# Kernel tuning notes

Measured on AMD Instinct MI355X. Metric: run time of the kernel, lower is better.

Reference implementation:

```python
import jax, jax.numpy as jnp
import numpy as np

# Dims: B=batch, C=in_ch (channels), L=pooled length, N=num_classes
B, C, L, N = 256, 2048, 512, 1000
FINAL_SHIFT = 4            # final_shift init arg
FC_SHIFT = 11              # int(log2(in_ch)) = int(log2(2048))


def dead_shift(x_i32, shift):
    # zero out values with |x| < 2^shift, then arithmetic right shift
    thr = jnp.int32(1 << shift)
    x = jnp.where(jnp.abs(x_i32) >= thr, x_i32, jnp.int32(0))
    return x >> shift  # numpy-style arithmetic shift for signed int32


def shift_clamp_i32_to_i8(x_i32, shift):
    x = dead_shift(x_i32, shift)
    return jnp.clip(x, -128, 127).astype(jnp.int8)


def setup_inputs() -> dict:
    key = jax.random.key(0)
    k1, k2 = jax.random.split(key)
    x = jax.random.randint(k1, (B, C, L), -128, 128, dtype=jnp.int32).astype(jnp.int8)
    weights = jax.random.randint(k2, (N, C), -128, 128, dtype=jnp.int32).astype(jnp.int8)
    return {"x": x, "weights": weights}


def reference(x, weights):
    # sum-pool over L: (B, C, L) -> (B, C) in int32
    acc = jnp.sum(x.astype(jnp.int32), axis=2)
    acc = dead_shift(acc, FINAL_SHIFT)
    # IntLinear: int32 matmul (same math as the torch broadcast-multiply-sum,
    # without materializing the (B, N, C) intermediate)
    w32 = weights.astype(jnp.int32)
    y = jnp.einsum('bc,nc->bn', acc, w32)  # (B, N) int32
    return shift_clamp_i32_to_i8(y, FC_SHIFT)
```

## Files before the change

### kernel.cpp

```cpp
#include <hip/hip_runtime.h>

#define BB 256
#define CC 2048
#define LL 512
#define NN 1000
#define FINAL_SHIFT 4
#define FC_SHIFT 11

#define TB 32
#define TN 64
#define BK 64

__device__ __forceinline__ int dead_shift_i(int x, int shift) {
    int thr = 1 << shift;
    int ax = x < 0 ? -x : x;
    x = (ax >= thr) ? x : 0;
    return x >> shift;
}

__global__ __launch_bounds__(256) void pool_kernel(const int* __restrict__ x,
                                                   int* __restrict__ acc) {
    int wave = threadIdx.x >> 6;
    int lane = threadIdx.x & 63;
    int g    = lane >> 4;
    int j    = lane & 15;
    long long rowBase = ((long long)blockIdx.x * 4 + wave) * 4;
    const int* p = x + (rowBase + g) * (long long)LL;

    int4 v[8];
#pragma unroll
    for (int c = 0; c < 8; ++c)
        v[c] = *(const int4*)(p + c * 64 + j * 4);

    int s = 0;
#pragma unroll
    for (int c = 0; c < 8; ++c) s += v[c].x + v[c].y + v[c].z + v[c].w;

    s += __shfl_xor(s, 1, 64);
    s += __shfl_xor(s, 2, 64);
    s += __shfl_xor(s, 4, 64);
    s += __shfl_xor(s, 8, 64);

    if (j == 0) acc[rowBase + g] = dead_shift_i(s, FINAL_SHIFT);
}

__global__ __launch_bounds__(256) void gemm_kernel(const int* __restrict__ acc,
                                                   const int* __restrict__ w,
                                                   int* __restrict__ partial,
                                                   int kch) {
    __shared__ int As[TB][BK + 1];
    __shared__ int Ws[BK][TN + 4];

    int b0 = blockIdx.x * TB;
    int n0 = blockIdx.y * TN;
    int kbase = blockIdx.z * kch;

    int t  = threadIdx.x;
    int tx = t & 15;
    int ty = t >> 4;

    int r[2][4] = {{0, 0, 0, 0}, {0, 0, 0, 0}};

    for (int k0 = kbase; k0 < kbase + kch; k0 += BK) {
        {
            int idx = t * 8;
            int b   = idx >> 6;
            int kk  = idx & 63;
            const int* src = acc + (long long)(b0 + b) * CC + k0 + kk;
            int4 u0 = *(const int4*)(src);
            int4 u1 = *(const int4*)(src + 4);
            As[b][kk + 0] = u0.x; As[b][kk + 1] = u0.y;
            As[b][kk + 2] = u0.z; As[b][kk + 3] = u0.w;
            As[b][kk + 4] = u1.x; As[b][kk + 5] = u1.y;
            As[b][kk + 6] = u1.z; As[b][kk + 7] = u1.w;
        }
#pragma unroll
        for (int rep = 0; rep < 4; ++rep) {
            int n  = rep * 16 + ty;
            int kk = tx * 4;
            int nn = n0 + n;
            int4 u = make_int4(0, 0, 0, 0);
            if (nn < NN) u = *(const int4*)(w + (long long)nn * CC + k0 + kk);
            Ws[kk + 0][n] = u.x; Ws[kk + 1][n] = u.y;
            Ws[kk + 2][n] = u.z; Ws[kk + 3][n] = u.w;
        }
        __syncthreads();

#pragma unroll
        for (int kk = 0; kk < BK; ++kk) {
            int4 wv = *(const int4*)&Ws[kk][tx * 4];
            int a0 = As[ty * 2 + 0][kk];
            int a1 = As[ty * 2 + 1][kk];
            r[0][0] += a0 * wv.x; r[0][1] += a0 * wv.y; r[0][2] += a0 * wv.z; r[0][3] += a0 * wv.w;
            r[1][0] += a1 * wv.x; r[1][1] += a1 * wv.y; r[1][2] += a1 * wv.z; r[1][3] += a1 * wv.w;
        }
        __syncthreads();
    }

    long long base = (long long)blockIdx.z * BB * NN;
#pragma unroll
    for (int i = 0; i < 2; ++i) {
#pragma unroll
        for (int j = 0; j < 4; ++j) {
            int n = n0 + tx * 4 + j;
            if (n < NN)
                partial[base + (long long)(b0 + ty * 2 + i) * NN + n] = r[i][j];
        }
    }
}

__global__ __launch_bounds__(256) void epilogue_kernel(const int* __restrict__ partial,
                                                       int* __restrict__ out, int z) {
    int idx = blockIdx.x * 256 + threadIdx.x;
    if (idx >= BB * NN) return;
    int s = 0;
    for (int i = 0; i < z; ++i) s += partial[(long long)i * BB * NN + idx];
    int v = dead_shift_i(s, FC_SHIFT);
    v = min(127, max(-128, v));
    out[idx] = v;
}

extern "C" void kernel_launch(void* const* d_in, const int* in_sizes, int n_in,
                              void* d_out, int out_size, void* d_ws, size_t ws_size,
                              hipStream_t stream) {
    const int* x = (const int*)d_in[0];
    const int* w = (const int*)d_in[1];
    int* out = (int*)d_out;

    int* acc     = (int*)d_ws;
    int* partial = acc + (size_t)BB * CC;

    size_t need4 = ((size_t)BB * CC + 4ull * BB * NN) * 4;
    int Z = (ws_size >= need4) ? 4 : 1;
    int kch = CC / Z;

    pool_kernel<<<(BB * CC) / 16, 256, 0, stream>>>(x, acc);

    dim3 g2(BB / TB, (NN + TN - 1) / TN, Z);
    gemm_kernel<<<g2, 256, 0, stream>>>(acc, w, partial, kch);

    epilogue_kernel<<<(BB * NN + 255) / 256, 256, 0, stream>>>(partial, out, Z);
}
```

Before: 236.1 us.

## Enlarge GEMM register tile, swizzle LDS, deepen split-K and double pool rows

The GEMM tile grows from 32x64 to 64x128, with a 4x8 per-thread register tile. A-tile stores to LDS are vectorised, and the W tile uses an XOR swizzle to reduce bank conflicts. Multiplies switch to __mul24, which is safe here because the pooled values and weights fit in 24 bits. Split-K now goes up to 16 chunks when workspace allows, and the pool kernel sums 8 rows per wave instead of 4 for more memory-level parallelism. The trade-off is more partial-sum traffic in the epilogue and higher register pressure in the GEMM.

```diff
diff --git a/kernel.cpp b/kernel.cpp
--- a/kernel.cpp
+++ b/kernel.cpp
@@ -7,9 +7,11 @@
 #define FINAL_SHIFT 4
 #define FC_SHIFT 11
 
-#define TB 32
-#define TN 64
+#define TBB 64
+#define TNN 128
 #define BK 64
+#define AP 76
+#define WP 132
 
 __device__ __forceinline__ int dead_shift_i(int x, int shift) {
     int thr = 1 << shift;
@@ -22,89 +24,128 @@
                                                    int* __restrict__ acc) {
     int wave = threadIdx.x >> 6;
     int lane = threadIdx.x & 63;
-    int g    = lane >> 4;
-    int j    = lane & 15;
-    long long rowBase = ((long long)blockIdx.x * 4 + wave) * 4;
-    const int* p = x + (rowBase + g) * (long long)LL;
+    int g = lane >> 4;
+    int j = lane & 15;
+    long long rowBase = ((long long)blockIdx.x * 4 + wave) * 8;
+    const int* pA = x + (rowBase + g) * (long long)LL;
+    const int* pB = x + (rowBase + 4 + g) * (long long)LL;
 
-    int4 v[8];
+    int4 v[8], u[8];
 #pragma unroll
-    for (int c = 0; c < 8; ++c)
-        v[c] = *(const int4*)(p + c * 64 + j * 4);
+    for (int c = 0; c < 8; ++c) v[c] = *(const int4*)(pA + c * 64 + j * 4);
+#pragma unroll
+    for (int c = 0; c < 8; ++c) u[c] = *(const int4*)(pB + c * 64 + j * 4);
 
-    int s = 0;
+    int sA = 0, sB = 0;
 #pragma unroll
-    for (int c = 0; c < 8; ++c) s += v[c].x + v[c].y + v[c].z + v[c].w;
+    for (int c = 0; c < 8; ++c) sA += v[c].x + v[c].y + v[c].z + v[c].w;
+#pragma unroll
+    for (int c = 0; c < 8; ++c) sB += u[c].x + u[c].y + u[c].z + u[c].w;
 
-    s += __shfl_xor(s, 1, 64);
-    s += __shfl_xor(s, 2, 64);
-    s += __shfl_xor(s, 4, 64);
-    s += __shfl_xor(s, 8, 64);
+    sA += __shfl_xor(sA, 1, 64);  sB += __shfl_xor(sB, 1, 64);
+    sA += __shfl_xor(sA, 2, 64);  sB += __shfl_xor(sB, 2, 64);
+    sA += __shfl_xor(sA, 4, 64);  sB += __shfl_xor(sB, 4, 64);
+    sA += __shfl_xor(sA, 8, 64);  sB += __shfl_xor(sB, 8, 64);
 
-    if (j == 0) acc[rowBase + g] = dead_shift_i(s, FINAL_SHIFT);
+    if (j == 0) {
+        acc[rowBase + g]     = dead_shift_i(sA, FINAL_SHIFT);
+        acc[rowBase + 4 + g] = dead_shift_i(sB, FINAL_SHIFT);
+    }
 }
 
 __global__ __launch_bounds__(256) void gemm_kernel(const int* __restrict__ acc,
                                                    const int* __restrict__ w,
                                                    int* __restrict__ partial,
                                                    int kch) {
-    __shared__ int As[TB][BK + 1];
-    __shared__ int Ws[BK][TN + 4];
+    __shared__ int As[TBB][AP];
+    __shared__ int Ws[BK][WP];
 
-    int b0 = blockIdx.x * TB;
-    int n0 = blockIdx.y * TN;
+    int b0 = blockIdx.x * TBB;
+    int n0 = blockIdx.y * TNN;
     int kbase = blockIdx.z * kch;
 
     int t  = threadIdx.x;
     int tx = t & 15;
     int ty = t >> 4;
 
-    int r[2][4] = {{0, 0, 0, 0}, {0, 0, 0, 0}};
+    int r[4][8];
+#pragma unroll
+    for (int bi = 0; bi < 4; ++bi)
+#pragma unroll
+        for (int j = 0; j < 8; ++j) r[bi][j] = 0;
 
     for (int k0 = kbase; k0 < kbase + kch; k0 += BK) {
         {
-            int idx = t * 8;
-            int b   = idx >> 6;
-            int kk  = idx & 63;
-            const int* src = acc + (long long)(b0 + b) * CC + k0 + kk;
-            int4 u0 = *(const int4*)(src);
+            int b  = t >> 2;
+            int kq = (t & 3) * 16;
+            const int* src = acc + (long long)(b0 + b) * CC + k0 + kq;
+            int4 u0 = *(const int4*)(src + 0);
             int4 u1 = *(const int4*)(src + 4);
-            As[b][kk + 0] = u0.x; As[b][kk + 1] = u0.y;
-            As[b][kk + 2] = u0.z; As[b][kk + 3] = u0.w;
-            As[b][kk + 4] = u1.x; As[b][kk + 5] = u1.y;
-            As[b][kk + 6] = u1.z; As[b][kk + 7] = u1.w;
+            int4 u2 = *(const int4*)(src + 8);
+            int4 u3 = *(const int4*)(src + 12);
+            *(int4*)&As[b][kq + 0]  = u0;
+            *(int4*)&As[b][kq + 4]  = u1;
+            *(int4*)&As[b][kq + 8]  = u2;
+            *(int4*)&As[b][kq + 12] = u3;
         }
+        {
+            int kk = tx * 4;
+            int sw = ((tx >> 1) & 3) << 2;
 #pragma unroll
-        for (int rep = 0; rep < 4; ++rep) {
-            int n  = rep * 16 + ty;
-            int kk = tx * 4;
-            int nn = n0 + n;
-            int4 u = make_int4(0, 0, 0, 0);
-            if (nn < NN) u = *(const int4*)(w + (long long)nn * CC + k0 + kk);
-            Ws[kk + 0][n] = u.x; Ws[kk + 1][n] = u.y;
-            Ws[kk + 2][n] = u.z; Ws[kk + 3][n] = u.w;
+            for (int rep = 0; rep < 8; ++rep) {
+                int n  = rep * 16 + ty;
+                int nn = n0 + n;
+                int4 uw = make_int4(0, 0, 0, 0);
+                if (nn < NN) uw = *(const int4*)(w + (long long)nn * CC + k0 + kk);
+                int c = n ^ sw;
+                Ws[kk + 0][c] = uw.x;
+                Ws[kk + 1][c] = uw.y;
+                Ws[kk + 2][c] = uw.z;
+                Ws[kk + 3][c] = uw.w;
+            }
         }
         __syncthreads();
 
 #pragma unroll
-        for (int kk = 0; kk < BK; ++kk) {
-            int4 wv = *(const int4*)&Ws[kk][tx * 4];
-            int a0 = As[ty * 2 + 0][kk];
-            int a1 = As[ty * 2 + 1][kk];
-            r[0][0] += a0 * wv.x; r[0][1] += a0 * wv.y; r[0][2] += a0 * wv.z; r[0][3] += a0 * wv.w;
-            r[1][0] += a1 * wv.x; r[1][1] += a1 * wv.y; r[1][2] += a1 * wv.z; r[1][3] += a1 * wv.w;
+        for (int kk4 = 0; kk4 < BK; kk4 += 4) {
+            int4 a[4];
+#pragma unroll
+            for (int bi = 0; bi < 4; ++bi)
+                a[bi] = *(const int4*)&As[ty * 4 + bi][kk4];
+#pragma unroll
+            for (int uu = 0; uu < 4; ++uu) {
+                int kk  = kk4 + uu;
+                int swr = ((kk >> 3) & 3) << 2;
+                int c0  = (tx * 4) ^ swr;
+                int4 w0 = *(const int4*)&Ws[kk][c0];
+                int4 w1 = *(const int4*)&Ws[kk][64 + c0];
+#pragma unroll
+                for (int bi = 0; bi < 4; ++bi) {
+                    int av = (uu == 0) ? a[bi].x : (uu == 1) ? a[bi].y
+                           : (uu == 2) ? a[bi].z : a[bi].w;
+                    r[bi][0] += __mul24(av, w0.x);
+                    r[bi][1] += __mul24(av, w0.y);
+                    r[bi][2] += __mul24(av, w0.z);
+                    r[bi][3] += __mul24(av, w0.w);
+                    r[bi][4] += __mul24(av, w1.x);
+                    r[bi][5] += __mul24(av, w1.y);
+                    r[bi][6] += __mul24(av, w1.z);
+                    r[bi][7] += __mul24(av, w1.w);
+                }
+            }
         }
         __syncthreads();
     }
 
     long long base = (long long)blockIdx.z * BB * NN;
 #pragma unroll
-    for (int i = 0; i < 2; ++i) {
+    for (int bi = 0; bi < 4; ++bi) {
+        int b = b0 + ty * 4 + bi;
 #pragma unroll
-        for (int j = 0; j < 4; ++j) {
-            int n = n0 + tx * 4 + j;
+        for (int j = 0; j < 8; ++j) {
+            int n = n0 + ((j < 4) ? (tx * 4 + j) : (64 + tx * 4 + (j - 4)));
             if (n < NN)
-                partial[base + (long long)(b0 + ty * 2 + i) * NN + n] = r[i][j];
+                partial[base + (long long)b * NN + n] = r[bi][j];
         }
     }
 }
@@ -130,13 +171,14 @@
     int* acc     = (int*)d_ws;
     int* partial = acc + (size_t)BB * CC;
 
-    size_t need4 = ((size_t)BB * CC + 4ull * BB * NN) * 4;
-    int Z = (ws_size >= need4) ? 4 : 1;
+    size_t accBytes = (size_t)BB * CC * 4;
+    int Z = 16;
+    while (Z > 1 && ws_size < accBytes + (size_t)Z * BB * NN * 4) Z >>= 1;
     int kch = CC / Z;
 
-    pool_kernel<<<(BB * CC) / 16, 256, 0, stream>>>(x, acc);
+    pool_kernel<<<(BB * CC) / 32, 256, 0, stream>>>(x, acc);
 
-    dim3 g2(BB / TB, (NN + TN - 1) / TN, Z);
+    dim3 g2(BB / TBB, (NN + TNN - 1) / TNN, Z);
     gemm_kernel<<<g2, 256, 0, stream>>>(acc, w, partial, kch);
 
     epilogue_kernel<<<(BB * NN + 255) / 256, 256, 0, stream>>>(partial, out, Z);
```

Result: no change. 232.7 us (-1.4%).
